# Kernel tuning notes

Hardware: AMD Instinct MI355X
Metric: run time of the kernel (lower is better)

The kernel has to match this reference:

```python
import math
import jax, jax.numpy as jnp
import numpy as np

B, N, D = 8, 1024, 1024
H, TKQ, TV = 16, 64, 64
DOUT = H * TV  # 1024, equals D
EPS = 1e-5


def _layer_norm(x, g, b):
    mu = jnp.mean(x, axis=-1, keepdims=True)
    var = jnp.mean((x - mu) ** 2, axis=-1, keepdims=True)
    return (x - mu) * jax.lax.rsqrt(var + EPS) * g + b


def setup_inputs() -> dict:
    key = jax.random.key(0)
    ks = jax.random.split(key, 16)
    s_w = 1.0 / math.sqrt(D)
    inp = {
        "tokens": jax.random.normal(ks[0], (B, N, D), jnp.float32),
        "Wq": jax.random.normal(ks[1], (H, D, TKQ), jnp.float32) * s_w,
        "bq": jax.random.uniform(ks[2], (H, 1, TKQ), jnp.float32, -s_w, s_w),
        "Wk": jax.random.normal(ks[3], (H, D, TKQ), jnp.float32) * s_w,
        "bk": jax.random.uniform(ks[4], (H, 1, TKQ), jnp.float32, -s_w, s_w),
        "Wv": jax.random.normal(ks[5], (H, D, TV), jnp.float32) * s_w,
        "bv": jax.random.uniform(ks[6], (H, 1, TV), jnp.float32, -s_w, s_w),
        "W1": jax.random.normal(ks[7], (DOUT, DOUT), jnp.float32) * (1.0 / math.sqrt(DOUT)),
        "b1": jax.random.uniform(ks[8], (DOUT,), jnp.float32, -s_w, s_w),
        "W2": jax.random.normal(ks[9], (DOUT, DOUT), jnp.float32) * (1.0 / math.sqrt(DOUT)),
        "b2": jax.random.uniform(ks[10], (DOUT,), jnp.float32, -s_w, s_w),
        "g1": jnp.ones((DOUT,), jnp.float32),
        "be1": jnp.zeros((DOUT,), jnp.float32),
        "g2": jnp.ones((DOUT,), jnp.float32),
        "be2": jnp.zeros((DOUT,), jnp.float32),
    }
    return inp


def reference(tokens, Wq, bq, Wk, bk, Wv, bv, W1, b1, W2, b2, g1, be1, g2, be2):
    # per-head projections: tokens[:,None] @ W + b  -> [B,H,N,T]
    tq = jnp.einsum("bnd,hdt->bhnt", tokens, Wq) + bq
    tk = jnp.einsum("bnd,hdt->bhnt", tokens, Wk) + bk
    tv = jnp.einsum("bnd,hdt->bhnt", tokens, Wv) + bv
    # non-standard scale: sqrt(num_heads * dim_tv)
    scale = math.sqrt(H * TV)
    scores = jnp.einsum("bhqt,bhkt->bhqk", tq, tk) / scale
    attn = jax.nn.softmax(scores, axis=-1)
    out = jnp.einsum("bhqk,bhkt->bhqt", attn, tv)  # [B,H,N,TV]
    # original flatten order: (B,N,TV,H) -> reshape(B,N,TV*H)
    out = jnp.transpose(out, (0, 2, 3, 1)).reshape(B, N, TV * H)
    # post-LN SAB path
    h = out + tokens
    h = _layer_norm(h, g1, be1)
    ff = jax.nn.relu(h @ W1 + b1) @ W2 + b2
    h = h + ff
    return _layer_norm(h, g2, be2)
```

## Files before the change

### kernel.cpp

```cpp
#include <hip/hip_runtime.h>
#include <hip/hip_bf16.h>

#define BB 8
#define NN_ 1024
#define DD 1024
#define HH 16
#define TT_ 64
#define MM (BB * NN_)

typedef __attribute__((ext_vector_type(8))) short short8;
typedef __attribute__((ext_vector_type(4))) float f32x4;
typedef __attribute__((ext_vector_type(4))) unsigned int u32x4;

__device__ __forceinline__ void g2lds16(const void* g, void* l) {
    __builtin_amdgcn_global_load_lds(
        (const __attribute__((address_space(1))) void*)g,
        (__attribute__((address_space(3))) void*)l, 16, 0, 0);
}

__device__ __forceinline__ __hip_bfloat16 f2b(float x) { return __float2bfloat16(x); }
__device__ __forceinline__ float b2f(unsigned short u) {
    unsigned v = (unsigned)u << 16;
    return __builtin_bit_cast(float, v);
}

__device__ __forceinline__ unsigned cvtpk(float a, float b) {
    unsigned r;
    asm("v_cvt_pk_bf16_f32 %0, %1, %2" : "=v"(r) : "v"(a), "v"(b));
    return r;
}

__global__ __launch_bounds__(256) void k_cvt_tokens(const float* __restrict__ in,
                                                    __hip_bfloat16* __restrict__ out) {
    int i = (blockIdx.x * 256 + threadIdx.x) * 4;
    float4 v = *(const float4*)&in[i];
    out[i + 0] = f2b(v.x); out[i + 1] = f2b(v.y);
    out[i + 2] = f2b(v.z); out[i + 3] = f2b(v.w);
}

__global__ __launch_bounds__(256) void k_cvt_wqkv(const float* __restrict__ Wq,
                                                  const float* __restrict__ Wk,
                                                  const float* __restrict__ Wv,
                                                  __hip_bfloat16* __restrict__ out) {
    __shared__ float tile[64][65];
    const int bid = blockIdx.x;
    const int proj = bid >> 8, h = (bid >> 4) & 15, dt = bid & 15;
    const float* W = proj == 0 ? Wq : (proj == 1 ? Wk : Wv);
    const float* src = W + ((size_t)h * 1024 + dt * 64) * 64;
    const int c = threadIdx.x & 63, r0 = threadIdx.x >> 6;
#pragma unroll
    for (int p = 0; p < 16; p++) {
        const int r = p * 4 + r0;
        tile[r][c] = src[(size_t)r * 64 + c];
    }
    __syncthreads();
    __hip_bfloat16* dst = out + (size_t)(proj * 1024 + h * 64) * 1024 + dt * 64;
#pragma unroll
    for (int p = 0; p < 16; p++) {
        const int r = p * 4 + r0;
        dst[(size_t)r * 1024 + c] = f2b(tile[c][r]);
    }
}

__global__ __launch_bounds__(256) void k_cvt_w(const float* __restrict__ W,
                                               __hip_bfloat16* __restrict__ out) {
    __shared__ float tile[64][65];
    const int ct = blockIdx.x & 15, dt = blockIdx.x >> 4;
    const float* src = W + (size_t)(dt * 64) * 1024 + ct * 64;
    const int c = threadIdx.x & 63, r0 = threadIdx.x >> 6;
#pragma unroll
    for (int p = 0; p < 16; p++) {
        const int r = p * 4 + r0;
        tile[r][c] = src[(size_t)r * 1024 + c];
    }
    __syncthreads();
    __hip_bfloat16* dst = out + (size_t)(ct * 64) * 1024 + dt * 64;
#pragma unroll
    for (int p = 0; p < 16; p++) {
        const int r = p * 4 + r0;
        dst[(size_t)r * 1024 + c] = f2b(tile[c][r]);
    }
}

template <int MODE>
__global__ __launch_bounds__(256) void k_gemm(
    const __hip_bfloat16* __restrict__ A, const __hip_bfloat16* __restrict__ Bt,
    const float* __restrict__ bias0, const float* __restrict__ bias1,
    const float* __restrict__ bias2,
    __hip_bfloat16* __restrict__ ob0, __hip_bfloat16* __restrict__ ob1,
    __hip_bfloat16* __restrict__ ob2,
    const __hip_bfloat16* __restrict__ res) {
    __shared__ __align__(16) __hip_bfloat16 As[2][128 * 64];
    __shared__ __align__(16) __hip_bfloat16 Bs[2][128 * 64];

    const int tid = threadIdx.x;
    const int wid = tid >> 6, lane = tid & 63;
    const int l15 = lane & 15, lhi = lane >> 4;
    const int wm = wid >> 1, wn = wid & 1;
    const int m0 = blockIdx.y * 128, n0 = blockIdx.x * 128;
    const int srow = lane >> 3;
    const int scol = ((lane & 7) ^ srow) * 8;

    const __hip_bfloat16* gsrc;
    if (wid < 2)
        gsrc = A + (size_t)(m0 + wid * 64 + srow) * 1024 + scol;
    else
        gsrc = Bt + (size_t)(n0 + (wid - 2) * 64 + srow) * 1024 + scol;
    const int lofs = (wid & 1) * 4096;

    auto stage = [&](int kt, int bufi) {
        __hip_bfloat16* lb = (wid < 2) ? &As[bufi][lofs] : &Bs[bufi][lofs];
#pragma unroll
        for (int i = 0; i < 8; ++i)
            g2lds16(gsrc + kt * 64 + (size_t)i * 8 * 1024, lb + i * 512);
    };

    f32x4 acc[4][4];
#pragma unroll
    for (int i = 0; i < 4; i++)
#pragma unroll
        for (int j = 0; j < 4; j++) acc[i][j] = (f32x4){0.f, 0.f, 0.f, 0.f};

    stage(0, 0);
    const int swz = l15 & 7;

    for (int kt = 0; kt < 16; ++kt) {
        const int cur = kt & 1;
        if (kt < 15) {
            stage(kt + 1, cur ^ 1);
            asm volatile("s_waitcnt vmcnt(8)" ::: "memory");
        } else {
            asm volatile("s_waitcnt vmcnt(0)" ::: "memory");
        }
        __builtin_amdgcn_s_barrier();
        asm volatile("" ::: "memory");
        __builtin_amdgcn_s_setprio(1);
#pragma unroll
        for (int kk = 0; kk < 2; ++kk) {
            const int ch = ((kk * 4 + lhi) ^ swz) * 8;
            short8 af[4], bfr[4];
#pragma unroll
            for (int mi = 0; mi < 4; mi++)
                af[mi] = *(const short8*)&As[cur][(wm * 64 + mi * 16 + l15) * 64 + ch];
#pragma unroll
            for (int ni = 0; ni < 4; ni++)
                bfr[ni] = *(const short8*)&Bs[cur][(wn * 64 + ni * 16 + l15) * 64 + ch];
#pragma unroll
            for (int mi = 0; mi < 4; mi++)
#pragma unroll
                for (int ni = 0; ni < 4; ni++)
                    acc[mi][ni] = __builtin_amdgcn_mfma_f32_16x16x32_bf16(
                        af[mi], bfr[ni], acc[mi][ni], 0, 0, 0);
        }
        __builtin_amdgcn_s_setprio(0);
        asm volatile("" ::: "memory");
        __builtin_amdgcn_s_barrier();
    }

#pragma unroll
    for (int mi = 0; mi < 4; mi++) {
#pragma unroll
        for (int ni = 0; ni < 4; ni++) {
            const int col = n0 + wn * 64 + ni * 16 + l15;
#pragma unroll
            for (int r = 0; r < 4; r++) {
                const int m = m0 + wm * 64 + mi * 16 + lhi * 4 + r;
                float v = acc[mi][ni][r];
                if (MODE == 0) {
                    const int proj = col >> 10, hh = (col >> 6) & 15, t = col & 63;
                    const float* bp = proj == 0 ? bias0 : (proj == 1 ? bias1 : bias2);
                    v += bp[hh * 64 + t];
                    const int b = m >> 10, n = m & 1023;
                    if (proj == 0)
                        ob0[((size_t)(b * 16 + hh) * 1024 + n) * 64 + t] = f2b(v * 0.04508422f);
                    else if (proj == 1)
                        ob1[((size_t)(b * 16 + hh) * 1024 + n) * 64 + t] = f2b(v);
                    else
                        ob2[((size_t)(b * 16 + hh) * 64 + t) * 1024 + n] = f2b(v);
                } else if (MODE == 1) {
                    v += bias0[col];
                    ob0[(size_t)m * 1024 + col] = f2b(fmaxf(v, 0.f));
                } else {
                    v += bias0[col] + b2f(*(const unsigned short*)&res[(size_t)m * 1024 + col]);
                    ob0[(size_t)m * 1024 + col] = f2b(v);
                }
            }
        }
    }
}

__global__ __launch_bounds__(256) void k_attn(const __hip_bfloat16* __restrict__ Q,
                                              const __hip_bfloat16* __restrict__ Kg,
                                              const __hip_bfloat16* __restrict__ Vt,
                                              __hip_bfloat16* __restrict__ attn_out) {
    __shared__ __align__(16) __hip_bfloat16 Ks[2][64 * 64];
    __shared__ __align__(16) __hip_bfloat16 Vs[2][64 * 64];

    const int tid = threadIdx.x, wid = tid >> 6, lane = tid & 63;
    const int l15 = lane & 15, lhi = lane >> 4;
    const int bid = blockIdx.x;
    const int qb = bid & 7, head = (bid >> 3) & 15, b = bid >> 7;
    const int bh = b * 16 + head;
    const __hip_bfloat16* Qg = Q + ((size_t)bh * 1024 + qb * 128) * 64;
    const __hip_bfloat16* Kp = Kg + (size_t)bh * 1024 * 64;
    const __hip_bfloat16* Vp = Vt + (size_t)bh * 64 * 1024;
    const int srow = lane >> 3;
    const int scol = ((lane & 7) ^ srow) * 8;

    auto stageKV = [&](int t, int bufi) {
#pragma unroll
        for (int i = 0; i < 2; i++) {
            const int krow = (wid * 2 + i) * 8 + srow;
            const int kperm = (krow & 0x23) | ((krow & 0x0C) << 1) | ((krow & 0x10) >> 2);
            g2lds16(Kp + (size_t)(t * 64 + kperm) * 64 + scol, &Ks[bufi][(wid * 2 + i) * 512]);
            g2lds16(Vp + (size_t)krow * 1024 + t * 64 + scol, &Vs[bufi][(wid * 2 + i) * 512]);
        }
    };
    stageKV(0, 0);

    short8 qf[2][2];
#pragma unroll
    for (int g = 0; g < 2; g++)
#pragma unroll
        for (int c = 0; c < 2; c++)
            qf[g][c] = *(const short8*)&Qg[(size_t)(wid * 32 + g * 16 + l15) * 64 + c * 32 + lhi * 8];

    f32x4 o[2][4];
#pragma unroll
    for (int g = 0; g < 2; g++)
#pragma unroll
        for (int i = 0; i < 4; i++) o[g][i] = (f32x4){0.f, 0.f, 0.f, 0.f};
    f32x4 lacc[2] = {(f32x4){0.f, 0.f, 0.f, 0.f}, (f32x4){0.f, 0.f, 0.f, 0.f}};
    const short bf16_one = (short)0x3F80;
    const short8 ones = (short8){bf16_one, bf16_one, bf16_one, bf16_one,
                                 bf16_one, bf16_one, bf16_one, bf16_one};

    const int sw = l15 & 7;
    const int c0 = (lhi ^ sw) * 8;

    for (int t = 0; t < 16; ++t) {
        const int cur = t & 1;
        if (t < 15) {
            stageKV(t + 1, cur ^ 1);
            asm volatile("s_waitcnt vmcnt(4)" ::: "memory");
        } else {
            asm volatile("s_waitcnt vmcnt(0)" ::: "memory");
        }
        __builtin_amdgcn_s_barrier();
        asm volatile("" ::: "memory");

        f32x4 s[2][4];
        __builtin_amdgcn_s_setprio(1);
#pragma unroll
        for (int nt = 0; nt < 4; ++nt) {
            const int kr = (nt * 16 + l15) * 64;
            short8 k0 = *(const short8*)&Ks[cur][kr + c0];
            short8 k1 = *(const short8*)&Ks[cur][kr + (c0 ^ 32)];
#pragma unroll
            for (int g = 0; g < 2; g++) {
                f32x4 z = (f32x4){0.f, 0.f, 0.f, 0.f};
                z = __builtin_amdgcn_mfma_f32_16x16x32_bf16(k0, qf[g][0], z, 0, 0, 0);
                s[g][nt] = __builtin_amdgcn_mfma_f32_16x16x32_bf16(k1, qf[g][1], z, 0, 0, 0);
            }
        }
        __builtin_amdgcn_s_setprio(0);

#pragma unroll
        for (int g = 0; g < 2; g++)
#pragma unroll
            for (int nt = 0; nt < 4; nt++)
#pragma unroll
                for (int r = 0; r < 4; r++) s[g][nt][r] = __builtin_exp2f(s[g][nt][r]);

        short8 pf[2][2];
#pragma unroll
        for (int g = 0; g < 2; g++) {
            u32x4 w0 = (u32x4){cvtpk(s[g][0][0], s[g][0][1]), cvtpk(s[g][0][2], s[g][0][3]),
                               cvtpk(s[g][1][0], s[g][1][1]), cvtpk(s[g][1][2], s[g][1][3])};
            u32x4 w1 = (u32x4){cvtpk(s[g][2][0], s[g][2][1]), cvtpk(s[g][2][2], s[g][2][3]),
                               cvtpk(s[g][3][0], s[g][3][1]), cvtpk(s[g][3][2], s[g][3][3])};
            pf[g][0] = __builtin_bit_cast(short8, w0);
            pf[g][1] = __builtin_bit_cast(short8, w1);
        }

        __builtin_amdgcn_s_setprio(1);
#pragma unroll
        for (int g = 0; g < 2; g++) {
            lacc[g] = __builtin_amdgcn_mfma_f32_16x16x32_bf16(pf[g][0], ones, lacc[g], 0, 0, 0);
            lacc[g] = __builtin_amdgcn_mfma_f32_16x16x32_bf16(pf[g][1], ones, lacc[g], 0, 0, 0);
        }
#pragma unroll
        for (int tt = 0; tt < 4; tt++) {
            const int vr = (tt * 16 + l15) * 64;
            short8 v0 = *(const short8*)&Vs[cur][vr + c0];
            short8 v1 = *(const short8*)&Vs[cur][vr + (c0 ^ 32)];
#pragma unroll
            for (int g = 0; g < 2; g++) {
                o[g][tt] = __builtin_amdgcn_mfma_f32_16x16x32_bf16(pf[g][0], v0, o[g][tt], 0, 0, 0);
                o[g][tt] = __builtin_amdgcn_mfma_f32_16x16x32_bf16(pf[g][1], v1, o[g][tt], 0, 0, 0);
            }
        }
        __builtin_amdgcn_s_setprio(0);
        asm volatile("" ::: "memory");
        __builtin_amdgcn_s_barrier();
    }

#pragma unroll
    for (int g = 0; g < 2; g++)
#pragma unroll
        for (int r = 0; r < 4; r++) {
            const float inv_r = 1.f / lacc[g][r];
            const int row = qb * 128 + wid * 32 + g * 16 + lhi * 4 + r;
#pragma unroll
            for (int tt = 0; tt < 4; tt++) {
                const int ch = (tt * 16 + l15) * 16 + head;
                attn_out[((size_t)(b * 1024 + row)) * 1024 + ch] = f2b(o[g][tt][r] * inv_r);
            }
        }
}

__global__ __launch_bounds__(256) void k_ln1(const __hip_bfloat16* __restrict__ x1,
                                             const float* __restrict__ x2,
                                             const float* __restrict__ g,
                                             const float* __restrict__ be,
                                             __hip_bfloat16* __restrict__ y) {
    const int row = blockIdx.x;
    const int tid = threadIdx.x, wid = tid >> 6, lane = tid & 63;
    const int c = tid * 4;
    const ushort4 u = *(const ushort4*)&x1[(size_t)row * 1024 + c];
    float4 xv;
    xv.x = b2f(u.x); xv.y = b2f(u.y); xv.z = b2f(u.z); xv.w = b2f(u.w);
    float4 a = *(const float4*)&x2[(size_t)row * 1024 + c];
    xv.x += a.x; xv.y += a.y; xv.z += a.z; xv.w += a.w;
    float s = xv.x + xv.y + xv.z + xv.w;
    float q = xv.x * xv.x + xv.y * xv.y + xv.z * xv.z + xv.w * xv.w;
#pragma unroll
    for (int msk = 1; msk < 64; msk <<= 1) {
        s += __shfl_xor(s, msk);
        q += __shfl_xor(q, msk);
    }
    __shared__ float ss[4], qq[4];
    if (lane == 0) { ss[wid] = s; qq[wid] = q; }
    __syncthreads();
    s = ss[0] + ss[1] + ss[2] + ss[3];
    q = qq[0] + qq[1] + qq[2] + qq[3];
    const float mu = s * (1.f / 1024.f);
    const float var = q * (1.f / 1024.f) - mu * mu;
    const float rs = rsqrtf(var + 1e-5f);
    float4 gv = *(const float4*)&g[c];
    float4 bv = *(const float4*)&be[c];
    __hip_bfloat16* d = y + (size_t)row * 1024 + c;
    d[0] = f2b((xv.x - mu) * rs * gv.x + bv.x);
    d[1] = f2b((xv.y - mu) * rs * gv.y + bv.y);
    d[2] = f2b((xv.z - mu) * rs * gv.z + bv.z);
    d[3] = f2b((xv.w - mu) * rs * gv.w + bv.w);
}

__global__ __launch_bounds__(256) void k_ln2(const __hip_bfloat16* __restrict__ x,
                                             const float* __restrict__ g,
                                             const float* __restrict__ be,
                                             float* __restrict__ y) {
    const int row = blockIdx.x;
    const int tid = threadIdx.x, wid = tid >> 6, lane = tid & 63;
    const int c = tid * 4;
    const ushort4 u = *(const ushort4*)&x[(size_t)row * 1024 + c];
    float4 xv;
    xv.x = b2f(u.x); xv.y = b2f(u.y); xv.z = b2f(u.z); xv.w = b2f(u.w);
    float s = xv.x + xv.y + xv.z + xv.w;
    float q = xv.x * xv.x + xv.y * xv.y + xv.z * xv.z + xv.w * xv.w;
#pragma unroll
    for (int msk = 1; msk < 64; msk <<= 1) {
        s += __shfl_xor(s, msk);
        q += __shfl_xor(q, msk);
    }
    __shared__ float ss[4], qq[4];
    if (lane == 0) { ss[wid] = s; qq[wid] = q; }
    __syncthreads();
    s = ss[0] + ss[1] + ss[2] + ss[3];
    q = qq[0] + qq[1] + qq[2] + qq[3];
    const float mu = s * (1.f / 1024.f);
    const float var = q * (1.f / 1024.f) - mu * mu;
    const float rs = rsqrtf(var + 1e-5f);
    float4 gv = *(const float4*)&g[c];
    float4 bv = *(const float4*)&be[c];
    float4 yv;
    yv.x = (xv.x - mu) * rs * gv.x + bv.x;
    yv.y = (xv.y - mu) * rs * gv.y + bv.y;
    yv.z = (xv.z - mu) * rs * gv.z + bv.z;
    yv.w = (xv.w - mu) * rs * gv.w + bv.w;
    *(float4*)&y[(size_t)row * 1024 + c] = yv;
}

extern "C" void kernel_launch(void* const* d_in, const int* in_sizes, int n_in,
                              void* d_out, int out_size, void* d_ws, size_t ws_size,
                              hipStream_t stream) {
    const float* tokens = (const float*)d_in[0];
    const float* Wq  = (const float*)d_in[1];
    const float* bq  = (const float*)d_in[2];
    const float* Wk  = (const float*)d_in[3];
    const float* bk  = (const float*)d_in[4];
    const float* Wv  = (const float*)d_in[5];
    const float* bv  = (const float*)d_in[6];
    const float* W1  = (const float*)d_in[7];
    const float* b1  = (const float*)d_in[8];
    const float* W2  = (const float*)d_in[9];
    const float* b2  = (const float*)d_in[10];
    const float* g1  = (const float*)d_in[11];
    const float* be1 = (const float*)d_in[12];
    const float* g2  = (const float*)d_in[13];
    const float* be2 = (const float*)d_in[14];

    char* ws = (char*)d_ws;
    const size_t MB = 1024 * 1024;
    __hip_bfloat16* tok_b  = (__hip_bfloat16*)(ws + 0);
    __hip_bfloat16* Wqkv_t = (__hip_bfloat16*)(ws + 16 * MB);
    __hip_bfloat16* W1t    = (__hip_bfloat16*)(ws + 22 * MB);
    __hip_bfloat16* W2t    = (__hip_bfloat16*)(ws + 24 * MB);
    __hip_bfloat16* Qb     = (__hip_bfloat16*)(ws + 26 * MB);
    __hip_bfloat16* Kb     = (__hip_bfloat16*)(ws + 42 * MB);
    __hip_bfloat16* Vtb    = (__hip_bfloat16*)(ws + 58 * MB);
    __hip_bfloat16* attn_b = (__hip_bfloat16*)(ws + 74 * MB);
    __hip_bfloat16* h1     = (__hip_bfloat16*)(ws + 90 * MB);
    __hip_bfloat16* t1     = (__hip_bfloat16*)(ws + 26 * MB);
    __hip_bfloat16* h2     = (__hip_bfloat16*)(ws + 42 * MB);

    k_cvt_tokens<<<8192, 256, 0, stream>>>(tokens, tok_b);
    k_cvt_wqkv<<<768, 256, 0, stream>>>(Wq, Wk, Wv, Wqkv_t);
    k_cvt_w<<<256, 256, 0, stream>>>(W1, W1t);
    k_cvt_w<<<256, 256, 0, stream>>>(W2, W2t);

    k_gemm<0><<<dim3(24, 64), 256, 0, stream>>>(tok_b, Wqkv_t, bq, bk, bv,
                                                Qb, Kb, Vtb, nullptr);
    k_attn<<<1024, 256, 0, stream>>>(Qb, Kb, Vtb, attn_b);
    k_ln1<<<8192, 256, 0, stream>>>(attn_b, tokens, g1, be1, h1);
    k_gemm<1><<<dim3(8, 64), 256, 0, stream>>>(h1, W1t, b1, nullptr, nullptr,
                                               t1, nullptr, nullptr, nullptr);
    k_gemm<2><<<dim3(8, 64), 256, 0, stream>>>(t1, W2t, b2, nullptr, nullptr,
                                               h2, nullptr, nullptr, h1);
    k_ln2<<<8192, 256, 0, stream>>>(h2, g2, be2, (float*)d_out);
}
```

Measured before the change: 251.2 us.

## Load K/V tiles directly into registers instead of staging through LDS

The attention kernel no longer stages K and V tiles into double-buffered shared memory with barriers. Each wave now loads its MFMA fragments straight from global memory into registers, prefetching the next tile while computing the current one, and the loop is fully unrolled. This removes the LDS round trip and the block-wide barriers. In exchange, the four waves in a block each re-read the same K/V data from global memory or cache, and register pressure rises from the extra prefetch buffers.

```diff
diff --git a/kernel.cpp b/kernel.cpp
--- a/kernel.cpp
+++ b/kernel.cpp
@@ -193,9 +193,6 @@
                                               const __hip_bfloat16* __restrict__ Kg,
                                               const __hip_bfloat16* __restrict__ Vt,
                                               __hip_bfloat16* __restrict__ attn_out) {
-    __shared__ __align__(16) __hip_bfloat16 Ks[2][64 * 64];
-    __shared__ __align__(16) __hip_bfloat16 Vs[2][64 * 64];
-
     const int tid = threadIdx.x, wid = tid >> 6, lane = tid & 63;
     const int l15 = lane & 15, lhi = lane >> 4;
     const int bid = blockIdx.x;
@@ -204,19 +201,16 @@
     const __hip_bfloat16* Qg = Q + ((size_t)bh * 1024 + qb * 128) * 64;
     const __hip_bfloat16* Kp = Kg + (size_t)bh * 1024 * 64;
     const __hip_bfloat16* Vp = Vt + (size_t)bh * 64 * 1024;
-    const int srow = lane >> 3;
-    const int scol = ((lane & 7) ^ srow) * 8;
-
-    auto stageKV = [&](int t, int bufi) {
-#pragma unroll
-        for (int i = 0; i < 2; i++) {
-            const int krow = (wid * 2 + i) * 8 + srow;
-            const int kperm = (krow & 0x23) | ((krow & 0x0C) << 1) | ((krow & 0x10) >> 2);
-            g2lds16(Kp + (size_t)(t * 64 + kperm) * 64 + scol, &Ks[bufi][(wid * 2 + i) * 512]);
-            g2lds16(Vp + (size_t)krow * 1024 + t * 64 + scol, &Vs[bufi][(wid * 2 + i) * 512]);
-        }
-    };
-    stageKV(0, 0);
+
+    const __hip_bfloat16* kb[4];
+    const __hip_bfloat16* vb[4];
+#pragma unroll
+    for (int nt = 0; nt < 4; nt++) {
+        const int i = nt * 16 + l15;
+        const int grow = (i & 0x23) | ((i & 0x0C) << 1) | ((i & 0x10) >> 2);
+        kb[nt] = Kp + (size_t)grow * 64 + lhi * 8;
+        vb[nt] = Vp + (size_t)(nt * 16 + l15) * 1024 + lhi * 8;
+    }
 
     short8 qf[2][2];
 #pragma unroll
@@ -235,32 +229,39 @@
     const short8 ones = (short8){bf16_one, bf16_one, bf16_one, bf16_one,
                                  bf16_one, bf16_one, bf16_one, bf16_one};
 
-    const int sw = l15 & 7;
-    const int c0 = (lhi ^ sw) * 8;
-
+    short8 kf[4][2], vf[4][2];
+#pragma unroll
+    for (int nt = 0; nt < 4; nt++) {
+        kf[nt][0] = *(const short8*)&kb[nt][0];
+        kf[nt][1] = *(const short8*)&kb[nt][32];
+        vf[nt][0] = *(const short8*)&vb[nt][0];
+        vf[nt][1] = *(const short8*)&vb[nt][32];
+    }
+
+#pragma unroll
     for (int t = 0; t < 16; ++t) {
-        const int cur = t & 1;
+        short8 kn[4][2], vn[4][2];
         if (t < 15) {
-            stageKV(t + 1, cur ^ 1);
-            asm volatile("s_waitcnt vmcnt(4)" ::: "memory");
-        } else {
-            asm volatile("s_waitcnt vmcnt(0)" ::: "memory");
-        }
-        __builtin_amdgcn_s_barrier();
-        asm volatile("" ::: "memory");
+#pragma unroll
+            for (int nt = 0; nt < 4; nt++) {
+                const __hip_bfloat16* kq = kb[nt] + (size_t)(t + 1) * 4096;
+                const __hip_bfloat16* vq = vb[nt] + (size_t)(t + 1) * 64;
+                kn[nt][0] = *(const short8*)&kq[0];
+                kn[nt][1] = *(const short8*)&kq[32];
+                vn[nt][0] = *(const short8*)&vq[0];
+                vn[nt][1] = *(const short8*)&vq[32];
+            }
+        }
 
         f32x4 s[2][4];
         __builtin_amdgcn_s_setprio(1);
 #pragma unroll
         for (int nt = 0; nt < 4; ++nt) {
-            const int kr = (nt * 16 + l15) * 64;
-            short8 k0 = *(const short8*)&Ks[cur][kr + c0];
-            short8 k1 = *(const short8*)&Ks[cur][kr + (c0 ^ 32)];
 #pragma unroll
             for (int g = 0; g < 2; g++) {
                 f32x4 z = (f32x4){0.f, 0.f, 0.f, 0.f};
-                z = __builtin_amdgcn_mfma_f32_16x16x32_bf16(k0, qf[g][0], z, 0, 0, 0);
-                s[g][nt] = __builtin_amdgcn_mfma_f32_16x16x32_bf16(k1, qf[g][1], z, 0, 0, 0);
+                z = __builtin_amdgcn_mfma_f32_16x16x32_bf16(kf[nt][0], qf[g][0], z, 0, 0, 0);
+                s[g][nt] = __builtin_amdgcn_mfma_f32_16x16x32_bf16(kf[nt][1], qf[g][1], z, 0, 0, 0);
             }
         }
         __builtin_amdgcn_s_setprio(0);
@@ -291,18 +292,21 @@
         }
 #pragma unroll
         for (int tt = 0; tt < 4; tt++) {
-            const int vr = (tt * 16 + l15) * 64;
-            short8 v0 = *(const short8*)&Vs[cur][vr + c0];
-            short8 v1 = *(const short8*)&Vs[cur][vr + (c0 ^ 32)];
 #pragma unroll
             for (int g = 0; g < 2; g++) {
-                o[g][tt] = __builtin_amdgcn_mfma_f32_16x16x32_bf16(pf[g][0], v0, o[g][tt], 0, 0, 0);
-                o[g][tt] = __builtin_amdgcn_mfma_f32_16x16x32_bf16(pf[g][1], v1, o[g][tt], 0, 0, 0);
+                o[g][tt] = __builtin_amdgcn_mfma_f32_16x16x32_bf16(pf[g][0], vf[tt][0], o[g][tt], 0, 0, 0);
+                o[g][tt] = __builtin_amdgcn_mfma_f32_16x16x32_bf16(pf[g][1], vf[tt][1], o[g][tt], 0, 0, 0);
             }
         }
         __builtin_amdgcn_s_setprio(0);
-        asm volatile("" ::: "memory");
-        __builtin_amdgcn_s_barrier();
+
+        if (t < 15) {
+#pragma unroll
+            for (int nt = 0; nt < 4; nt++) {
+                kf[nt][0] = kn[nt][0]; kf[nt][1] = kn[nt][1];
+                vf[nt][0] = vn[nt][0]; vf[nt][1] = vn[nt][1];
+            }
+        }
     }
 
 #pragma unroll
```

After: 307.1 us. 1.22x slower.
